# Kernel tuning notes

Measured on AMD Instinct MI355X. Metric: run time of the kernel, lower is better.

## Reference

```python
import jax, jax.numpy as jnp
import numpy as np

N = 100000      # nodes
E = 1200000     # directed edges (before self loops)
IN = 128        # in_channels
POS = 16        # pos_dim
H = 4           # heads
OUT = 16        # out_channels per head
NEG_SLOPE = 0.2
DIV_W = 0.1


def setup_inputs() -> dict:
    key = jax.random.key(0)
    k0, k1, k2, k3, k4 = jax.random.split(key, 5)
    x = jax.random.normal(k0, (N, IN), jnp.float32)
    edge_index = jax.random.randint(k1, (2, E), 0, N, dtype=jnp.int64)
    W = jax.random.normal(k2, (IN - POS, H * OUT), jnp.float32) * (1.0 / np.sqrt(IN - POS).astype(np.float32))
    att = jax.random.normal(k3, (1, H, 2 * OUT), jnp.float32) * 0.1
    pos_att = jax.random.normal(k4, (1, H, 2 * POS), jnp.float32) * 0.1
    bias = jnp.zeros((H * OUT,), jnp.float32)
    return {"x": x, "edge_index": edge_index, "W": W, "att": att, "pos_att": pos_att, "bias": bias}


def _segment_softmax(scores, seg, n):
    # numerically stable softmax over segments defined by seg (per source node, as in the torch code)
    m = jax.ops.segment_max(scores, seg, num_segments=n)           # [n, H]
    e = jnp.exp(scores - m[seg])                                   # [E', H]
    s = jax.ops.segment_sum(e, seg, num_segments=n)                # [n, H]
    return e / (s[seg] + 1e-10)


def _diversity_loss(alpha):
    # pairwise correlations between L2-normalized per-head attention vectors,
    # diagonal left at zero, mean over full HxH matrix (matches torch loop)
    norm = jnp.maximum(jnp.linalg.norm(alpha, axis=0, keepdims=True), 1e-12)
    a = alpha / norm                                               # [E', H]
    gram = a.T @ a                                                 # [H, H]
    gram = gram * (1.0 - jnp.eye(H, dtype=gram.dtype))
    return jnp.mean(gram) * DIV_W


def reference(x, edge_index, W, att, pos_att, bias):
    n = x.shape[0]
    loops = jnp.arange(n, dtype=edge_index.dtype)
    row = jnp.concatenate([edge_index[0], loops])                  # [E'] = E + N
    col = jnp.concatenate([edge_index[1], loops])

    content = (x[:, :-POS] @ W).reshape(n, H, OUT)                 # [n, H, OUT]
    pos = x[:, -POS:]                                              # [n, POS]

    # concat([c_i, c_j]) . att == c_i . att[:OUT] + c_j . att[OUT:]  (compute per-node, gather per-edge)
    s_ci = jnp.einsum('nhd,hd->nh', content, att[0, :, :OUT])
    s_cj = jnp.einsum('nhd,hd->nh', content, att[0, :, OUT:])
    s_pi = pos @ pos_att[0, :, :POS].T                             # [n, H]
    s_pj = pos @ pos_att[0, :, POS:].T

    alpha = (s_ci + s_pi)[row] + (s_cj + s_pj)[col]                # [E', H]
    alpha = jax.nn.leaky_relu(alpha, NEG_SLOPE)
    alpha = _segment_softmax(alpha, row, n)

    diversity_loss = _diversity_loss(alpha)

    # message: x_j * alpha (x_j = content[source] = content[row]); aggregate: scatter-add at target (col)
    msgs = content[row] * alpha[:, :, None]                        # [E', H, OUT]
    out = jax.ops.segment_sum(msgs, col, num_segments=n)           # [n, H, OUT]
    out = out.reshape(n, H * OUT) + bias
    return (out, diversity_loss)
```

## Files before the change

kernel.cpp:

```cpp
#include <hip/hip_runtime.h>
#include <hip/hip_fp16.h>

#define NN   100000
#define NE   1200000
#define MT   (NE + NN)
#define HH   4
#define HD   64
#define NEG_SLOPE 0.2f
#define NGB  25000
#define SBLK 1024
#define EPB  1270
#define NCB  782
#define NBKT 392
#define BCAP 4096

static __device__ __forceinline__ unsigned short f2bf(float f) {
    unsigned int b = __float_as_uint(f);
    b += 0x7FFFu + ((b >> 16) & 1u);
    return (unsigned short)(b >> 16);
}
static __device__ __forceinline__ float h_lo(unsigned w) {
    return __half2float(__ushort_as_half((unsigned short)(w & 0xffff)));
}
static __device__ __forceinline__ float h_hi(unsigned w) {
    return __half2float(__ushort_as_half((unsigned short)(w >> 16)));
}
static __device__ __forceinline__ unsigned pack_h2(float a, float b) {
    return (unsigned)__half_as_ushort(__float2half(a)) |
           ((unsigned)__half_as_ushort(__float2half(b)) << 16);
}

__global__ __launch_bounds__(256) void k_fused(
    const float* __restrict__ x, const float* __restrict__ W,
    const float* __restrict__ att, const float* __restrict__ pos_att,
    const int* __restrict__ ei,
    unsigned* __restrict__ regionD, unsigned* __restrict__ regionR,
    unsigned short* __restrict__ offD16, unsigned short* __restrict__ offR16,
    unsigned short* __restrict__ contentb, __half* __restrict__ nd,
    __half* __restrict__ sjh)
{
    __shared__ __align__(16) char smem[45056];
    const int t = threadIdx.x;

    if (blockIdx.x < SBLK) {
        unsigned* scan = (unsigned*)smem;
        unsigned* curs = (unsigned*)(smem + 4096);
        unsigned* stD  = (unsigned*)(smem + 7232);
        unsigned* stR  = (unsigned*)(smem + 12352);
        const int p  = blockIdx.x;
        const int e0 = p * EPB;
        const int e1 = min(e0 + EPB, MT);
        for (int i = t; i < 1024; i += 256) scan[i] = 0;
        __syncthreads();
        int er[5], ec[5];
        #pragma unroll
        for (int k = 0; k < 5; ++k) {
            const int e = e0 + t + k * 256;
            if (e < e1) {
                int r, c;
                if (e < NE) {
                    r = __builtin_nontemporal_load(ei + e);
                    c = __builtin_nontemporal_load(ei + NE + e);
                } else { r = e - NE; c = r; }
                er[k] = r; ec[k] = c;
                atomicAdd(&scan[c >> 8], 1u);
                atomicAdd(&scan[512 + (r >> 8)], 1u);
            } else er[k] = -1;
        }
        __syncthreads();
        for (int s = 1; s < 1024; s <<= 1) {
            unsigned v[4];
            #pragma unroll
            for (int k = 0; k < 4; ++k) {
                const int i = t + k * 256;
                v[k] = (i >= s) ? scan[i - s] : 0u;
            }
            __syncthreads();
            #pragma unroll
            for (int k = 0; k < 4; ++k) scan[t + k * 256] += v[k];
            __syncthreads();
        }
        const unsigned totD  = scan[511];
        const unsigned base_ = scan[511];
        const unsigned totR  = scan[1023] - base_;
        for (int i = t; i < NBKT; i += 256) {
            const unsigned dstart = (i == 0) ? 0u : scan[i - 1];
            const unsigned rstart = ((i == 0) ? base_ : scan[512 + i - 1]) - base_;
            curs[i]        = dstart;
            curs[392 + i]  = rstart;
            offD16[(size_t)p * (NBKT + 1) + i] = (unsigned short)dstart;
            offR16[(size_t)p * (NBKT + 1) + i] = (unsigned short)rstart;
        }
        if (t == 0) {
            offD16[(size_t)p * (NBKT + 1) + NBKT] = (unsigned short)totD;
            offR16[(size_t)p * (NBKT + 1) + NBKT] = (unsigned short)totR;
        }
        __syncthreads();
        #pragma unroll
        for (int k = 0; k < 5; ++k) {
            if (er[k] >= 0) {
                const unsigned pd = atomicAdd(&curs[ec[k] >> 8], 1u);
                stD[pd] = (unsigned)er[k] | ((unsigned)(ec[k] & 255) << 17);
                const unsigned pr = atomicAdd(&curs[392 + (er[k] >> 8)], 1u);
                stR[pr] = (unsigned)ec[k] | ((unsigned)(er[k] & 255) << 17);
            }
        }
        __syncthreads();
        for (unsigned i = t; i < totD; i += 256)
            regionD[(size_t)p * EPB + i] = stD[i];
        for (unsigned i = t; i < totR; i += 256)
            regionR[(size_t)p * EPB + i] = stR[i];
        return;
    }

    float* Wl  = (float*)smem;
    float* xsT = (float*)(smem + 28672);
    for (int i = t; i < 112 * 64; i += 256) Wl[i] = W[i];

    const int gb  = blockIdx.x - SBLK;
    const int n0  = gb * 128;
    const int oc  = (t & 7) * 8;
    const int h   = oc >> 4;
    const int ng4 = (t >> 3) * 4;

    float acc[4][8];
    #pragma unroll
    for (int j = 0; j < 4; ++j)
        #pragma unroll
        for (int o = 0; o < 8; ++o) acc[j][o] = 0.f;

    for (int ph = 0; ph < 4; ++ph) {
        __syncthreads();
        for (int idx = t; idx < 128 * 32; idx += 256) {
            const int nl = idx >> 5;
            const int kk = idx & 31;
            const int gn = n0 + nl;
            const float v = (gn < NN) ? x[(size_t)gn * 128 + ph * 32 + kk] : 0.f;
            xsT[kk * 128 + (nl ^ (kk << 2))] = v;
        }
        __syncthreads();
        const int klim = (ph == 3) ? 16 : 32;
        #pragma unroll 4
        for (int kk = 0; kk < klim; ++kk) {
            const int sw = kk << 2;
            const float4 xv = *(const float4*)&xsT[kk * 128 + (ng4 ^ sw)];
            const int kg = ph * 32 + kk;
            const float4 w0 = *(const float4*)&Wl[kg * 64 + oc];
            const float4 w1 = *(const float4*)&Wl[kg * 64 + oc + 4];
            const float xa[4] = { xv.x, xv.y, xv.z, xv.w };
            #pragma unroll
            for (int j = 0; j < 4; ++j) {
                acc[j][0] = fmaf(xa[j], w0.x, acc[j][0]);
                acc[j][1] = fmaf(xa[j], w0.y, acc[j][1]);
                acc[j][2] = fmaf(xa[j], w0.z, acc[j][2]);
                acc[j][3] = fmaf(xa[j], w0.w, acc[j][3]);
                acc[j][4] = fmaf(xa[j], w1.x, acc[j][4]);
                acc[j][5] = fmaf(xa[j], w1.y, acc[j][5]);
                acc[j][6] = fmaf(xa[j], w1.z, acc[j][6]);
                acc[j][7] = fmaf(xa[j], w1.w, acc[j][7]);
            }
        }
    }

    const int dbase = oc & 15;
    float ati[8], atj[8], pti[8], ptj[8];
    #pragma unroll
    for (int j = 0; j < 8; ++j) {
        ati[j] = att[h * 32 + dbase + j];
        atj[j] = att[h * 32 + 16 + dbase + j];
        pti[j] = pos_att[h * 32 + dbase + j];
        ptj[j] = pos_att[h * 32 + 16 + dbase + j];
    }
    #pragma unroll
    for (int j = 0; j < 4; ++j) {
        const int gn = n0 + ng4 + j;
        float s1 = 0.f, s2 = 0.f;
        #pragma unroll
        for (int o = 0; o < 8; ++o) {
            s1 = fmaf(acc[j][o], ati[o], s1);
            s2 = fmaf(acc[j][o], atj[o], s2);
        }
        #pragma unroll
        for (int pp = 0; pp < 8; ++pp) {
            const int r3 = 16 + dbase + pp;
            const float pv = xsT[r3 * 128 + ((ng4 + j) ^ (r3 << 2))];
            s1 = fmaf(pv, pti[pp], s1);
            s2 = fmaf(pv, ptj[pp], s2);
        }
        s1 += __shfl_xor(s1, 1);
        s2 += __shfl_xor(s2, 1);
        if (gn < NN) {
            if ((t & 1) == 0) nd[(size_t)gn * 8 + h]  = __float2half(s1);
            else              sjh[(size_t)gn * 4 + h] = __float2half(s2);
            uint4 pk;
            pk.x = (unsigned)f2bf(acc[j][0]) | ((unsigned)f2bf(acc[j][1]) << 16);
            pk.y = (unsigned)f2bf(acc[j][2]) | ((unsigned)f2bf(acc[j][3]) << 16);
            pk.z = (unsigned)f2bf(acc[j][4]) | ((unsigned)f2bf(acc[j][5]) << 16);
            pk.w = (unsigned)f2bf(acc[j][6]) | ((unsigned)f2bf(acc[j][7]) << 16);
            *(uint4*)&contentb[(size_t)gn * 64 + oc] = pk;
        }
    }
}

__global__ __launch_bounds__(256) void k_pass2(
    const unsigned* __restrict__ regionD, const unsigned* __restrict__ regionR,
    const unsigned short* __restrict__ offD16, const unsigned short* __restrict__ offR16,
    __half* __restrict__ nd, const __half* __restrict__ sjh,
    unsigned* __restrict__ sortedC, int* __restrict__ nodeoff,
    int* __restrict__ nodedeg, int* __restrict__ btot)
{
    __shared__ __align__(16) char smem[35328];
    const int t = threadIdx.x;

    if (blockIdx.x < NBKT) {
        const int g = blockIdx.x;
        unsigned* cnt   = (unsigned*)smem;
        unsigned* curs  = (unsigned*)(smem + 1024);
        unsigned* rawc  = (unsigned*)(smem + 2048);
        unsigned* raw   = (unsigned*)(smem + 2560);
        unsigned* srt   = (unsigned*)(smem + 2560 + BCAP * 4);
        cnt[t] = 0;
        if (t == 0) rawc[0] = 0;
        __syncthreads();
        for (int pb = t; pb < SBLK; pb += 256) {
            const int o0 = offD16[(size_t)pb * (NBKT + 1) + g];
            const int o1 = offD16[(size_t)pb * (NBKT + 1) + g + 1];
            const int s  = o1 - o0;
            if (s > 0) {
                const unsigned base = atomicAdd(rawc, (unsigned)s);
                if (base + s <= BCAP) {
                    for (int i = 0; i < s; ++i) {
                        const unsigned rec = regionD[(size_t)pb * EPB + o0 + i];
                        raw[base + i] = rec;
                        atomicAdd(&cnt[rec >> 17], 1u);
                    }
                }
            }
        }
        __syncthreads();
        const unsigned total = min(rawc[0], (unsigned)BCAP);
        curs[t] = cnt[t];
        __syncthreads();
        for (int s = 1; s < 256; s <<= 1) {
            const unsigned v = (t >= s) ? curs[t - s] : 0u;
            __syncthreads();
            curs[t] += v;
            __syncthreads();
        }
        const unsigned start = curs[t] - cnt[t];
        const int node = g * 256 + t;
        if (node < NN) {
            nodeoff[node] = g * BCAP + (int)start;
            nodedeg[node] = (int)cnt[t];
        }
        if (t == 0) btot[g] = (int)total;
        __syncthreads();
        curs[t] = start;
        __syncthreads();
        for (unsigned i = t; i < total; i += 256) {
            const unsigned rec = raw[i];
            const unsigned pos = atomicAdd(&curs[rec >> 17], 1u);
            srt[pos] = rec;
        }
        __syncthreads();
        for (unsigned i = t; i < total; i += 256)
            sortedC[(size_t)g * BCAP + i] = srt[i];
        return;
    }

    const int g = blockIdx.x - NBKT;
    float* den = (float*)smem;
    float* siL = (float*)(smem + 4096);
    for (int i = t; i < 1024; i += 256) den[i] = 0.f;
    const int node = g * 256 + t;
    if (node < NN) {
        const uint2 sv = *(const uint2*)(nd + (size_t)node * 8);
        siL[t * 4 + 0] = h_lo(sv.x); siL[t * 4 + 1] = h_hi(sv.x);
        siL[t * 4 + 2] = h_lo(sv.y); siL[t * 4 + 3] = h_hi(sv.y);
    } else {
        siL[t * 4 + 0] = 0.f; siL[t * 4 + 1] = 0.f;
        siL[t * 4 + 2] = 0.f; siL[t * 4 + 3] = 0.f;
    }
    __syncthreads();
    for (int pb = t; pb < SBLK; pb += 256) {
        const int o0 = offR16[(size_t)pb * (NBKT + 1) + g];
        const int o1 = offR16[(size_t)pb * (NBKT + 1) + g + 1];
        for (int i = o0; i < o1; ++i) {
            const unsigned rec = regionR[(size_t)pb * EPB + i];
            const int c    = (int)(rec & 0x1FFFFu);
            const int lrow = (int)(rec >> 17);
            const uint2 jv = *(const uint2*)(sjh + (size_t)c * 4);
            float v0 = siL[lrow * 4 + 0] + h_lo(jv.x);
            float v1 = siL[lrow * 4 + 1] + h_hi(jv.x);
            float v2 = siL[lrow * 4 + 2] + h_lo(jv.y);
            float v3 = siL[lrow * 4 + 3] + h_hi(jv.y);
            v0 = v0 > 0.f ? v0 : NEG_SLOPE * v0;
            v1 = v1 > 0.f ? v1 : NEG_SLOPE * v1;
            v2 = v2 > 0.f ? v2 : NEG_SLOPE * v2;
            v3 = v3 > 0.f ? v3 : NEG_SLOPE * v3;
            atomicAdd(&den[lrow * 4 + 0], __expf(v0));
            atomicAdd(&den[lrow * 4 + 1], __expf(v1));
            atomicAdd(&den[lrow * 4 + 2], __expf(v2));
            atomicAdd(&den[lrow * 4 + 3], __expf(v3));
        }
    }
    __syncthreads();
    if (node < NN) {
        uint2 dv;
        dv.x = (unsigned)__half_as_ushort(__float2half(den[t * 4 + 0])) |
               ((unsigned)__half_as_ushort(__float2half(den[t * 4 + 1])) << 16);
        dv.y = (unsigned)__half_as_ushort(__float2half(den[t * 4 + 2])) |
               ((unsigned)__half_as_ushort(__float2half(den[t * 4 + 3])) << 16);
        *(uint2*)(nd + (size_t)node * 8 + 4) = dv;
    }
}

__global__ __launch_bounds__(256) void k_alpha(
    const unsigned* __restrict__ sortedC, const int* __restrict__ btot,
    const __half* __restrict__ nd, const __half* __restrict__ sjh,
    uint2* __restrict__ sortedA, float* __restrict__ gpart)
{
    __shared__ uint2 sjL[256];
    __shared__ float red[4][10];
    const int t = threadIdx.x;
    const int g = blockIdx.x >> 2;
    const int q = blockIdx.x & 3;
    const int node = g * 256 + t;
    uint2 z; z.x = 0; z.y = 0;
    sjL[t] = (node < NN) ? *(const uint2*)(sjh + (size_t)node * 4) : z;
    __syncthreads();
    const int total = btot[g];
    float a0=0,a1=0,a2=0,a3=0,a4=0,a5=0,a6=0,a7=0,a8=0,a9=0;
    for (int i = q * 256 + t; i < total; i += 1024) {
        const unsigned rec = sortedC[(size_t)g * BCAP + i];
        const int r    = (int)(rec & 0x1FFFFu);
        const int lrow = (int)(rec >> 17);
        const uint4 nr = *(const uint4*)(nd + (size_t)r * 8);
        const uint2 jv = sjL[lrow];
        float v0 = h_lo(nr.x) + h_lo(jv.x);
        float v1 = h_hi(nr.x) + h_hi(jv.x);
        float v2 = h_lo(nr.y) + h_lo(jv.y);
        float v3 = h_hi(nr.y) + h_hi(jv.y);
        v0 = v0 > 0.f ? v0 : NEG_SLOPE * v0;
        v1 = v1 > 0.f ? v1 : NEG_SLOPE * v1;
        v2 = v2 > 0.f ? v2 : NEG_SLOPE * v2;
        v3 = v3 > 0.f ? v3 : NEG_SLOPE * v3;
        const float al0 = __expf(v0) / (h_lo(nr.z) + 1e-10f);
        const float al1 = __expf(v1) / (h_hi(nr.z) + 1e-10f);
        const float al2 = __expf(v2) / (h_lo(nr.w) + 1e-10f);
        const float al3 = __expf(v3) / (h_hi(nr.w) + 1e-10f);
        uint2 aw;
        aw.x = pack_h2(al0, al1);
        aw.y = pack_h2(al2, al3);
        sortedA[(size_t)g * BCAP + i] = aw;
        a0=fmaf(al0,al0,a0); a1=fmaf(al0,al1,a1); a2=fmaf(al0,al2,a2); a3=fmaf(al0,al3,a3);
        a4=fmaf(al1,al1,a4); a5=fmaf(al1,al2,a5); a6=fmaf(al1,al3,a6);
        a7=fmaf(al2,al2,a7); a8=fmaf(al2,al3,a8); a9=fmaf(al3,al3,a9);
    }
    #pragma unroll
    for (int m = 32; m >= 1; m >>= 1) {
        a0 += __shfl_xor(a0, m); a1 += __shfl_xor(a1, m);
        a2 += __shfl_xor(a2, m); a3 += __shfl_xor(a3, m);
        a4 += __shfl_xor(a4, m); a5 += __shfl_xor(a5, m);
        a6 += __shfl_xor(a6, m); a7 += __shfl_xor(a7, m);
        a8 += __shfl_xor(a8, m); a9 += __shfl_xor(a9, m);
    }
    const int lane = t & 63, wid = t >> 6;
    if (lane == 0) {
        red[wid][0]=a0; red[wid][1]=a1; red[wid][2]=a2; red[wid][3]=a3; red[wid][4]=a4;
        red[wid][5]=a5; red[wid][6]=a6; red[wid][7]=a7; red[wid][8]=a8; red[wid][9]=a9;
    }
    __syncthreads();
    if (t < 10)
        gpart[(size_t)blockIdx.x * 10 + t] =
            red[0][t] + red[1][t] + red[2][t] + red[3][t];
}

__global__ __launch_bounds__(256) void k_gather(
    const int* __restrict__ nodeoff, const int* __restrict__ nodedeg,
    const unsigned* __restrict__ sortedC, const uint2* __restrict__ sortedA,
    const unsigned short* __restrict__ contentb, const float* __restrict__ bias,
    float* __restrict__ out)
{
    const int lane = threadIdx.x & 63;
    const int wid  = threadIdx.x >> 6;
    const int n    = blockIdx.x * 4 + wid;
    const int h    = lane >> 4;
    const int start = nodeoff[n];
    const int cd    = min(nodedeg[n], 64);
    float acc = 0.f;

    const int rl = (lane < cd) ? (int)(sortedC[(size_t)start + lane] & 0x1FFFFu) : 0;
    int j = 0;
    for (; j + 7 < cd; j += 8) {
        int rk[8];
        uint2 aw[8];
        float cv[8];
        #pragma unroll
        for (int k = 0; k < 8; ++k) rk[k] = __shfl(rl, j + k);
        #pragma unroll
        for (int k = 0; k < 8; ++k) aw[k] = sortedA[(size_t)start + j + k];
        #pragma unroll
        for (int k = 0; k < 8; ++k)
            cv[k] = __uint_as_float((unsigned)contentb[(size_t)rk[k] * 64 + lane] << 16);
        #pragma unroll
        for (int k = 0; k < 8; ++k) {
            const unsigned w = (h & 2) ? aw[k].y : aw[k].x;
            const float al = (h & 1) ? h_hi(w) : h_lo(w);
            acc = fmaf(cv[k], al, acc);
        }
    }
    for (; j < cd; ++j) {
        const int rk = __shfl(rl, j);
        const uint2 aw = sortedA[(size_t)start + j];
        const unsigned w = (h & 2) ? aw.y : aw.x;
        const float al = (h & 1) ? h_hi(w) : h_lo(w);
        const float cvv = __uint_as_float((unsigned)contentb[(size_t)rk * 64 + lane] << 16);
        acc = fmaf(cvv, al, acc);
    }
    out[(size_t)n * 64 + lane] = acc + bias[lane];
}

__global__ __launch_bounds__(256) void k_gred(
    const float* __restrict__ gpart, double* __restrict__ pairs)
{
    const int row = blockIdx.x * 256 + threadIdx.x;
    float v[10];
    #pragma unroll
    for (int i = 0; i < 10; ++i)
        v[i] = (row < 4 * NBKT) ? gpart[(size_t)row * 10 + i] : 0.f;
    #pragma unroll
    for (int m = 32; m >= 1; m >>= 1)
        #pragma unroll
        for (int i = 0; i < 10; ++i) v[i] += __shfl_xor(v[i], m);
    __shared__ float red[4][10];
    const int lane = threadIdx.x & 63, wid = threadIdx.x >> 6;
    if (lane == 0)
        #pragma unroll
        for (int i = 0; i < 10; ++i) red[wid][i] = v[i];
    __syncthreads();
    if (threadIdx.x < 10) {
        const double s = (double)red[0][threadIdx.x] + red[1][threadIdx.x]
                       + red[2][threadIdx.x] + red[3][threadIdx.x];
        atomicAdd(pairs + threadIdx.x, s);
    }
}

__global__ void k_loss(const double* __restrict__ ps, float* __restrict__ out)
{
    if (threadIdx.x == 0 && blockIdx.x == 0) {
        const double s00=ps[0], s01=ps[1], s02=ps[2], s03=ps[3], s11=ps[4];
        const double s12=ps[5], s13=ps[6], s22=ps[7], s23=ps[8], s33=ps[9];
        const double n0 = fmax(sqrt(s00), 1e-12);
        const double n1 = fmax(sqrt(s11), 1e-12);
        const double n2 = fmax(sqrt(s22), 1e-12);
        const double n3 = fmax(sqrt(s33), 1e-12);
        double loss = 2.0 * ( s01/(n0*n1) + s02/(n0*n2) + s03/(n0*n3)
                            + s12/(n1*n2) + s13/(n1*n3) + s23/(n2*n3) );
        loss = loss / 16.0 * 0.1;
        out[NN * HD] = (float)loss;
    }
}

extern "C" void kernel_launch(void* const* d_in, const int* in_sizes, int n_in,
                              void* d_out, int out_size, void* d_ws, size_t ws_size,
                              hipStream_t stream)
{
    const float* x       = (const float*)d_in[0];
    const int*   ei      = (const int*)d_in[1];
    const float* W       = (const float*)d_in[2];
    const float* att     = (const float*)d_in[3];
    const float* pos_att = (const float*)d_in[4];
    const float* bias    = (const float*)d_in[5];
    float* out = (float*)d_out;

    char* p = (char*)d_ws;
    double* pairs = (double*)p;              p += 128;
    __half* nd    = (__half*)p;              p += (size_t)NN * 8 * 2;
    __half* sjh   = (__half*)p;              p += (size_t)NN * 4 * 2;
    float*  gpart = (float*)p;               p += (size_t)4 * NBKT * 10 * 4 + 64;
    unsigned short* contentb = (unsigned short*)p; p += (size_t)NN * 64 * 2;
    unsigned* regionD = (unsigned*)p;        p += (size_t)SBLK * EPB * 4;
    unsigned* regionR = (unsigned*)p;        p += (size_t)SBLK * EPB * 4;
    unsigned short* offD16 = (unsigned short*)p; p += (size_t)SBLK * (NBKT+1) * 2;
    unsigned short* offR16 = (unsigned short*)p; p += (size_t)SBLK * (NBKT+1) * 2;
    unsigned* sortedC = (unsigned*)p;        p += (size_t)NBKT * BCAP * 4;
    uint2*   sortedA = (uint2*)p;            p += (size_t)NBKT * BCAP * 8;
    int* nodeoff = (int*)p;                  p += (size_t)NN * 4;
    int* nodedeg = (int*)p;                  p += (size_t)NN * 4;
    int* btot    = (int*)p;                  p += (size_t)NBKT * 4 + 64;

    (void)hipMemsetAsync(pairs, 0, 128, stream);

    k_fused <<<SBLK + NCB, 256, 0, stream>>>(x, W, att, pos_att, ei,
                                             regionD, regionR, offD16, offR16,
                                             contentb, nd, sjh);
    k_pass2 <<<2 * NBKT, 256, 0, stream>>>(regionD, regionR, offD16, offR16,
                                           nd, sjh, sortedC, nodeoff, nodedeg, btot);
    k_alpha <<<4 * NBKT, 256, 0, stream>>>(sortedC, btot, nd, sjh, sortedA, gpart);
    k_gather<<<NGB, 256, 0, stream>>>(nodeoff, nodedeg, sortedC, sortedA,
                                      contentb, bias, out);
    k_gred  <<<(4 * NBKT + 255) / 256, 256, 0, stream>>>(gpart, pairs);
    k_loss  <<<1, 64, 0, stream>>>(pairs, out);
}
```

Before: 309.3 us.

## Halve bucket width to 128 nodes and load gather records directly

Doubles the number of node buckets (128 nodes each, capacity 2048 edges), so pass2 and alpha kernels launch twice as many smaller blocks with less shared memory and better occupancy/parallelism. Scan arrays and offsets in the partition kernel grow accordingly, and the alpha kernel uses two quarters per bucket instead of four. The gather kernel now reads edge records per unrolled step instead of shuffling a preloaded lane value, with readfirstlane on offsets. Risks: more per-partition offset entries to scan, half the threads idle in pass2 sections, and bucket overflow at the smaller cap.

```diff
diff --git a/kernel.cpp b/kernel.cpp
--- a/kernel.cpp
+++ b/kernel.cpp
@@ -11,8 +11,8 @@
 #define SBLK 1024
 #define EPB  1270
 #define NCB  782
-#define NBKT 392
-#define BCAP 4096
+#define NBKT 782
+#define BCAP 2048
 
 static __device__ __forceinline__ unsigned short f2bf(float f) {
     unsigned int b = __float_as_uint(f);
@@ -44,13 +44,13 @@
 
     if (blockIdx.x < SBLK) {
         unsigned* scan = (unsigned*)smem;
-        unsigned* curs = (unsigned*)(smem + 4096);
-        unsigned* stD  = (unsigned*)(smem + 7232);
-        unsigned* stR  = (unsigned*)(smem + 12352);
+        unsigned* curs = (unsigned*)(smem + 8192);
+        unsigned* stD  = (unsigned*)(smem + 14448);
+        unsigned* stR  = (unsigned*)(smem + 19568);
         const int p  = blockIdx.x;
         const int e0 = p * EPB;
         const int e1 = min(e0 + EPB, MT);
-        for (int i = t; i < 1024; i += 256) scan[i] = 0;
+        for (int i = t; i < 2048; i += 256) scan[i] = 0;
         __syncthreads();
         int er[5], ec[5];
         #pragma unroll
@@ -63,31 +63,31 @@
                     c = __builtin_nontemporal_load(ei + NE + e);
                 } else { r = e - NE; c = r; }
                 er[k] = r; ec[k] = c;
-                atomicAdd(&scan[c >> 8], 1u);
-                atomicAdd(&scan[512 + (r >> 8)], 1u);
+                atomicAdd(&scan[c >> 7], 1u);
+                atomicAdd(&scan[1024 + (r >> 7)], 1u);
             } else er[k] = -1;
         }
         __syncthreads();
-        for (int s = 1; s < 1024; s <<= 1) {
-            unsigned v[4];
+        for (int s = 1; s < 2048; s <<= 1) {
+            unsigned v[8];
             #pragma unroll
-            for (int k = 0; k < 4; ++k) {
+            for (int k = 0; k < 8; ++k) {
                 const int i = t + k * 256;
                 v[k] = (i >= s) ? scan[i - s] : 0u;
             }
             __syncthreads();
             #pragma unroll
-            for (int k = 0; k < 4; ++k) scan[t + k * 256] += v[k];
+            for (int k = 0; k < 8; ++k) scan[t + k * 256] += v[k];
             __syncthreads();
         }
-        const unsigned totD  = scan[511];
-        const unsigned base_ = scan[511];
-        const unsigned totR  = scan[1023] - base_;
+        const unsigned totD  = scan[1023];
+        const unsigned base_ = scan[1023];
+        const unsigned totR  = scan[2047] - base_;
         for (int i = t; i < NBKT; i += 256) {
             const unsigned dstart = (i == 0) ? 0u : scan[i - 1];
-            const unsigned rstart = ((i == 0) ? base_ : scan[512 + i - 1]) - base_;
-            curs[i]        = dstart;
-            curs[392 + i]  = rstart;
+            const unsigned rstart = ((i == 0) ? base_ : scan[1024 + i - 1]) - base_;
+            curs[i]         = dstart;
+            curs[NBKT + i]  = rstart;
             offD16[(size_t)p * (NBKT + 1) + i] = (unsigned short)dstart;
             offR16[(size_t)p * (NBKT + 1) + i] = (unsigned short)rstart;
         }
@@ -99,10 +99,10 @@
         #pragma unroll
         for (int k = 0; k < 5; ++k) {
             if (er[k] >= 0) {
-                const unsigned pd = atomicAdd(&curs[ec[k] >> 8], 1u);
-                stD[pd] = (unsigned)er[k] | ((unsigned)(ec[k] & 255) << 17);
-                const unsigned pr = atomicAdd(&curs[392 + (er[k] >> 8)], 1u);
-                stR[pr] = (unsigned)ec[k] | ((unsigned)(er[k] & 255) << 17);
+                const unsigned pd = atomicAdd(&curs[ec[k] >> 7], 1u);
+                stD[pd] = (unsigned)er[k] | ((unsigned)(ec[k] & 127) << 17);
+                const unsigned pr = atomicAdd(&curs[NBKT + (er[k] >> 7)], 1u);
+                stR[pr] = (unsigned)ec[k] | ((unsigned)(er[k] & 127) << 17);
             }
         }
         __syncthreads();
@@ -209,17 +209,17 @@
     unsigned* __restrict__ sortedC, int* __restrict__ nodeoff,
     int* __restrict__ nodedeg, int* __restrict__ btot)
 {
-    __shared__ __align__(16) char smem[35328];
+    __shared__ __align__(16) char smem[17920];
     const int t = threadIdx.x;
 
     if (blockIdx.x < NBKT) {
         const int g = blockIdx.x;
         unsigned* cnt   = (unsigned*)smem;
-        unsigned* curs  = (unsigned*)(smem + 1024);
-        unsigned* rawc  = (unsigned*)(smem + 2048);
-        unsigned* raw   = (unsigned*)(smem + 2560);
-        unsigned* srt   = (unsigned*)(smem + 2560 + BCAP * 4);
-        cnt[t] = 0;
+        unsigned* curs  = (unsigned*)(smem + 512);
+        unsigned* rawc  = (unsigned*)(smem + 1024);
+        unsigned* raw   = (unsigned*)(smem + 1536);
+        unsigned* srt   = (unsigned*)(smem + 1536 + BCAP * 4);
+        if (t < 128) cnt[t] = 0;
         if (t == 0) rawc[0] = 0;
         __syncthreads();
         for (int pb = t; pb < SBLK; pb += 256) {
@@ -239,23 +239,25 @@
         }
         __syncthreads();
         const unsigned total = min(rawc[0], (unsigned)BCAP);
-        curs[t] = cnt[t];
-        __syncthreads();
-        for (int s = 1; s < 256; s <<= 1) {
-            const unsigned v = (t >= s) ? curs[t - s] : 0u;
+        if (t < 128) curs[t] = cnt[t];
+        __syncthreads();
+        for (int s = 1; s < 128; s <<= 1) {
+            unsigned v = 0;
+            if (t < 128 && t >= s) v = curs[t - s];
             __syncthreads();
-            curs[t] += v;
+            if (t < 128) curs[t] += v;
             __syncthreads();
         }
-        const unsigned start = curs[t] - cnt[t];
-        const int node = g * 256 + t;
-        if (node < NN) {
-            nodeoff[node] = g * BCAP + (int)start;
-            nodedeg[node] = (int)cnt[t];
+        if (t < 128) {
+            const unsigned start = curs[t] - cnt[t];
+            const int node = g * 128 + t;
+            if (node < NN) {
+                nodeoff[node] = g * BCAP + (int)start;
+                nodedeg[node] = (int)cnt[t];
+            }
+            curs[t] = start;
         }
         if (t == 0) btot[g] = (int)total;
-        __syncthreads();
-        curs[t] = start;
         __syncthreads();
         for (unsigned i = t; i < total; i += 256) {
             const unsigned rec = raw[i];
@@ -270,16 +272,18 @@
 
     const int g = blockIdx.x - NBKT;
     float* den = (float*)smem;
-    float* siL = (float*)(smem + 4096);
-    for (int i = t; i < 1024; i += 256) den[i] = 0.f;
-    const int node = g * 256 + t;
-    if (node < NN) {
-        const uint2 sv = *(const uint2*)(nd + (size_t)node * 8);
-        siL[t * 4 + 0] = h_lo(sv.x); siL[t * 4 + 1] = h_hi(sv.x);
-        siL[t * 4 + 2] = h_lo(sv.y); siL[t * 4 + 3] = h_hi(sv.y);
-    } else {
-        siL[t * 4 + 0] = 0.f; siL[t * 4 + 1] = 0.f;
-        siL[t * 4 + 2] = 0.f; siL[t * 4 + 3] = 0.f;
+    float* siL = (float*)(smem + 2048);
+    for (int i = t; i < 512; i += 256) den[i] = 0.f;
+    if (t < 128) {
+        const int node = g * 128 + t;
+        if (node < NN) {
+            const uint2 sv = *(const uint2*)(nd + (size_t)node * 8);
+            siL[t * 4 + 0] = h_lo(sv.x); siL[t * 4 + 1] = h_hi(sv.x);
+            siL[t * 4 + 2] = h_lo(sv.y); siL[t * 4 + 3] = h_hi(sv.y);
+        } else {
+            siL[t * 4 + 0] = 0.f; siL[t * 4 + 1] = 0.f;
+            siL[t * 4 + 2] = 0.f; siL[t * 4 + 3] = 0.f;
+        }
     }
     __syncthreads();
     for (int pb = t; pb < SBLK; pb += 256) {
@@ -305,13 +309,14 @@
         }
     }
     __syncthreads();
-    if (node < NN) {
-        uint2 dv;
-        dv.x = (unsigned)__half_as_ushort(__float2half(den[t * 4 + 0])) |
-               ((unsigned)__half_as_ushort(__float2half(den[t * 4 + 1])) << 16);
-        dv.y = (unsigned)__half_as_ushort(__float2half(den[t * 4 + 2])) |
-               ((unsigned)__half_as_ushort(__float2half(den[t * 4 + 3])) << 16);
-        *(uint2*)(nd + (size_t)node * 8 + 4) = dv;
+    if (t < 128) {
+        const int node = g * 128 + t;
+        if (node < NN) {
+            uint2 dv;
+            dv.x = pack_h2(den[t * 4 + 0], den[t * 4 + 1]);
+            dv.y = pack_h2(den[t * 4 + 2], den[t * 4 + 3]);
+            *(uint2*)(nd + (size_t)node * 8 + 4) = dv;
+        }
     }
 }
 
@@ -320,18 +325,20 @@
     const __half* __restrict__ nd, const __half* __restrict__ sjh,
     uint2* __restrict__ sortedA, float* __restrict__ gpart)
 {
-    __shared__ uint2 sjL[256];
+    __shared__ uint2 sjL[128];
     __shared__ float red[4][10];
     const int t = threadIdx.x;
-    const int g = blockIdx.x >> 2;
-    const int q = blockIdx.x & 3;
-    const int node = g * 256 + t;
-    uint2 z; z.x = 0; z.y = 0;
-    sjL[t] = (node < NN) ? *(const uint2*)(sjh + (size_t)node * 4) : z;
+    const int g = blockIdx.x >> 1;
+    const int q = blockIdx.x & 1;
+    if (t < 128) {
+        const int node = g * 128 + t;
+        uint2 z; z.x = 0; z.y = 0;
+        sjL[t] = (node < NN) ? *(const uint2*)(sjh + (size_t)node * 4) : z;
+    }
     __syncthreads();
     const int total = btot[g];
     float a0=0,a1=0,a2=0,a3=0,a4=0,a5=0,a6=0,a7=0,a8=0,a9=0;
-    for (int i = q * 256 + t; i < total; i += 1024) {
+    for (int i = q * 256 + t; i < total; i += 512) {
         const unsigned rec = sortedC[(size_t)g * BCAP + i];
         const int r    = (int)(rec & 0x1FFFFu);
         const int lrow = (int)(rec >> 17);
@@ -386,23 +393,23 @@
     const int wid  = threadIdx.x >> 6;
     const int n    = blockIdx.x * 4 + wid;
     const int h    = lane >> 4;
-    const int start = nodeoff[n];
-    const int cd    = min(nodedeg[n], 64);
+    const int start = __builtin_amdgcn_readfirstlane(nodeoff[n]);
+    const int cd    = __builtin_amdgcn_readfirstlane(min(nodedeg[n], 64));
     float acc = 0.f;
 
-    const int rl = (lane < cd) ? (int)(sortedC[(size_t)start + lane] & 0x1FFFFu) : 0;
     int j = 0;
     for (; j + 7 < cd; j += 8) {
-        int rk[8];
+        unsigned rec[8];
         uint2 aw[8];
         float cv[8];
         #pragma unroll
-        for (int k = 0; k < 8; ++k) rk[k] = __shfl(rl, j + k);
+        for (int k = 0; k < 8; ++k) rec[k] = sortedC[(size_t)start + j + k];
         #pragma unroll
         for (int k = 0; k < 8; ++k) aw[k] = sortedA[(size_t)start + j + k];
         #pragma unroll
         for (int k = 0; k < 8; ++k)
-            cv[k] = __uint_as_float((unsigned)contentb[(size_t)rk[k] * 64 + lane] << 16);
+            cv[k] = __uint_as_float(
+                (unsigned)contentb[(size_t)(rec[k] & 0x1FFFFu) * 64 + lane] << 16);
         #pragma unroll
         for (int k = 0; k < 8; ++k) {
             const unsigned w = (h & 2) ? aw[k].y : aw[k].x;
@@ -411,11 +418,12 @@
         }
     }
     for (; j < cd; ++j) {
-        const int rk = __shfl(rl, j);
+        const unsigned rec = sortedC[(size_t)start + j];
         const uint2 aw = sortedA[(size_t)start + j];
         const unsigned w = (h & 2) ? aw.y : aw.x;
         const float al = (h & 1) ? h_hi(w) : h_lo(w);
-        const float cvv = __uint_as_float((unsigned)contentb[(size_t)rk * 64 + lane] << 16);
+        const float cvv = __uint_as_float(
+            (unsigned)contentb[(size_t)(rec & 0x1FFFFu) * 64 + lane] << 16);
         acc = fmaf(cvv, al, acc);
     }
     out[(size_t)n * 64 + lane] = acc + bias[lane];
@@ -428,7 +436,7 @@
     float v[10];
     #pragma unroll
     for (int i = 0; i < 10; ++i)
-        v[i] = (row < 4 * NBKT) ? gpart[(size_t)row * 10 + i] : 0.f;
+        v[i] = (row < 2 * NBKT) ? gpart[(size_t)row * 10 + i] : 0.f;
     #pragma unroll
     for (int m = 32; m >= 1; m >>= 1)
         #pragma unroll
@@ -478,7 +486,7 @@
     double* pairs = (double*)p;              p += 128;
     __half* nd    = (__half*)p;              p += (size_t)NN * 8 * 2;
     __half* sjh   = (__half*)p;              p += (size_t)NN * 4 * 2;
-    float*  gpart = (float*)p;               p += (size_t)4 * NBKT * 10 * 4 + 64;
+    float*  gpart = (float*)p;               p += (size_t)2 * NBKT * 10 * 4 + 64;
     unsigned short* contentb = (unsigned short*)p; p += (size_t)NN * 64 * 2;
     unsigned* regionD = (unsigned*)p;        p += (size_t)SBLK * EPB * 4;
     unsigned* regionR = (unsigned*)p;        p += (size_t)SBLK * EPB * 4;
@@ -497,9 +505,9 @@
                                              contentb, nd, sjh);
     k_pass2 <<<2 * NBKT, 256, 0, stream>>>(regionD, regionR, offD16, offR16,
                                            nd, sjh, sortedC, nodeoff, nodedeg, btot);
-    k_alpha <<<4 * NBKT, 256, 0, stream>>>(sortedC, btot, nd, sjh, sortedA, gpart);
+    k_alpha <<<2 * NBKT, 256, 0, stream>>>(sortedC, btot, nd, sjh, sortedA, gpart);
     k_gather<<<NGB, 256, 0, stream>>>(nodeoff, nodedeg, sortedC, sortedA,
                                       contentb, bias, out);
-    k_gred  <<<(4 * NBKT + 255) / 256, 256, 0, stream>>>(gpart, pairs);
+    k_gred  <<<(2 * NBKT + 255) / 256, 256, 0, stream>>>(gpart, pairs);
     k_loss  <<<1, 64, 0, stream>>>(pairs, out);
 }
```

New measurement: 278.8 us. 1.11x faster.
